# Kernel optimization log

Hardware: AMD Instinct MI355X
Metric: run time of the kernel (lower is better)

## Reference

```python
import jax, jax.numpy as jnp
import numpy as np

# FP4 e2m1 lookup: nibble -> value (bit3 = sign, bits2:0 = e2m1 magnitude)
FP4_LUT = jnp.array([0.0, 0.5, 1.0, 1.5, 2.0, 3.0, 4.0, 6.0,
                     -0.0, -0.5, -1.0, -1.5, -2.0, -3.0, -4.0, -6.0], dtype=jnp.float32)
BLOCK = 16  # elements per micro-scale (one uint8 E8M0 scale per 16 fp4 values)


def _dequant(packed, sf):
    """packed: [R, K//2] int bytes (two fp4 nibbles each, low nibble first).
    sf: [R, K//16] E8M0 exponents (value = 2^(sf-127)). Returns [R, K] f32."""
    R, Kh = packed.shape
    K = Kh * 2
    lo = packed & 0xF
    hi = (packed >> 4) & 0xF
    nib = jnp.stack([lo, hi], axis=-1).reshape(R, K)
    vals = FP4_LUT[nib]  # [R, K]
    block_scale = jnp.exp2((sf - 127).astype(jnp.float32))  # [R, K//16]
    return (vals.reshape(R, K // BLOCK, BLOCK) * block_scale[:, :, None]).reshape(R, K)


def setup_inputs() -> dict:
    key = jax.random.key(0)
    ks = jax.random.split(key, 6)
    M, N, K = 8192, 4096, 4224  # K = in_features(4096) + select_num(128)
    A_packed = jax.random.randint(ks[0], (M, K // 2), 0, 256, dtype=jnp.int32)
    SFA = jax.random.randint(ks[1], (M, K // BLOCK), 118, 134, dtype=jnp.int32)
    B_packed = jax.random.randint(ks[2], (N, K // 2), 0, 256, dtype=jnp.int32)
    SFB = jax.random.randint(ks[3], (N, K // BLOCK), 118, 134, dtype=jnp.int32)
    scale = jax.random.uniform(ks[4], (1,), dtype=jnp.float32, minval=0.5, maxval=1.5)
    bias = jax.random.normal(ks[5], (N,), dtype=jnp.float32)
    return {"A_packed": A_packed, "SFA": SFA, "scale": scale,
            "B_packed": B_packed, "SFB": SFB, "bias": bias}


def reference(A_packed, SFA, scale, B_packed, SFB, bias):
    A = _dequant(A_packed, SFA)        # [M, K]
    B = _dequant(B_packed, SFB)        # [N, K]
    # y = scale * (A @ B^T) + bias   (self.scale == 1.0 folded into scale)
    y = scale[0] * jnp.einsum('mk,nk->mn', A, B) + bias[None, :]
    return y
```

## Files before the change

kernel.cpp:

```cpp
#include <hip/hip_runtime.h>
#include <stdint.h>

#define M_DIM 8192
#define N_DIM 4096
#define K_DIM 4224
#define BK 64

typedef float f32x16 __attribute__((ext_vector_type(16)));
typedef int   i32x8  __attribute__((ext_vector_type(8)));
typedef int   i32x4  __attribute__((ext_vector_type(4)));

#define RAW_BARRIER()  asm volatile("s_barrier" ::: "memory")
#define WAIT_VM4()     asm volatile("s_waitcnt vmcnt(4)" ::: "memory")
#define WAIT_VM0()     asm volatile("s_waitcnt vmcnt(0)" ::: "memory")

__device__ __forceinline__ uint32_t conv4(uint32_t x, uint32_t k1) {
    uint32_t n7   = x & 0x07070707u;
    uint32_t base = __builtin_amdgcn_perm(0x46444240u, 0x3E3C3800u, n7);
    uint32_t nz   = __builtin_amdgcn_perm(0x01010101u, 0x01010100u, n7);
    uint32_t sign = (x & 0x08080808u) << 4;
    return (base + nz * k1 - (nz << 6)) | sign;
}

__global__ __launch_bounds__(256) void dequant_all(
    const int* __restrict__ Ap, const int* __restrict__ SFA, uint8_t* __restrict__ Aout,
    const int* __restrict__ Bp, const int* __restrict__ SFB, uint8_t* __restrict__ Bout)
{
    const int nblkA = M_DIM * K_DIM / 16;
    int i = blockIdx.x * 256 + threadIdx.x;
    const int* p; const int* sf; uint8_t* out; int idx;
    if (i < nblkA) { p = Ap; sf = SFA; out = Aout; idx = i; }
    else           { p = Bp; sf = SFB; out = Bout; idx = i - nblkA; }

    const int4* p4 = (const int4*)p;
    int4 p0 = p4[2 * idx];
    int4 p1 = p4[2 * idx + 1];
    int s4 = (sf[idx] - 127) << 2;
    uint32_t k1 = (uint32_t)(s4 + 64);

    uint32_t o[4];
#pragma unroll
    for (int g = 0; g < 2; ++g) {
        int4 pg = g ? p1 : p0;
        uint32_t w = (uint32_t)(pg.x & 0xFF) | ((uint32_t)(pg.y & 0xFF) << 8) |
                     ((uint32_t)(pg.z & 0xFF) << 16) | ((uint32_t)pg.w << 24);
        uint32_t lr = conv4(w & 0x0F0F0F0Fu, k1);
        uint32_t hr = conv4((w >> 4) & 0x0F0F0F0Fu, k1);
        o[2 * g]     = __builtin_amdgcn_perm(hr, lr, 0x05010400u);
        o[2 * g + 1] = __builtin_amdgcn_perm(hr, lr, 0x07030602u);
    }
    *(uint4*)(out + (size_t)idx * 16) = make_uint4(o[0], o[1], o[2], o[3]);
}

__global__ __launch_bounds__(512, 2) void gemm_mx(
    const uint8_t* __restrict__ A, const uint8_t* __restrict__ B,
    const float* __restrict__ scale, const float* __restrict__ bias,
    float* __restrict__ C)
{
    __shared__ uint8_t smem[98304];

    const int tid  = threadIdx.x;
    const int lane = tid & 63;
    const int w    = tid >> 6;
    const int wm   = w >> 2;
    const int wn   = w & 3;
    const int r31  = lane & 31;
    const int h    = lane >> 5;

    const int lin = blockIdx.y * 16 + blockIdx.x;
    const int o   = (lin & 7) * 64 + (lin >> 3);
    const int bn0 = (o & 15) * 256;
    const int bm0 = (o >> 4) * 256;

    f32x16 acc[4][2];
#pragma unroll
    for (int i = 0; i < 4; ++i)
#pragma unroll
        for (int j = 0; j < 2; ++j)
            acc[i][j] = (f32x16)(0.0f);

    const int srow = lane >> 2;
    const int scol = (((lane & 3) ^ ((lane >> 3) & 3)) << 4);
    const uint8_t* Ag = A + (size_t)(bm0 + w * 32 + srow) * K_DIM + scol;
    const uint8_t* Bg = B + (size_t)(bn0 + w * 32 + srow) * K_DIM + scol;
    uint8_t* Asw = smem + w * 2048;
    uint8_t* Bsw = smem + 16384 + w * 2048;

#define STAGE(koff, boff)                                                        \
    do {                                                                         \
        const uint8_t* ag_ = Ag + (koff);                                        \
        const uint8_t* bg_ = Bg + (koff);                                        \
        __builtin_amdgcn_global_load_lds(                                        \
            (const __attribute__((address_space(1))) void*)(ag_),                \
            (__attribute__((address_space(3))) void*)(Asw + (boff)), 16, 0, 0);  \
        __builtin_amdgcn_global_load_lds(                                        \
            (const __attribute__((address_space(1))) void*)(ag_ + (size_t)16 * K_DIM), \
            (__attribute__((address_space(3))) void*)(Asw + (boff) + 1024), 16, 0, 0); \
        __builtin_amdgcn_global_load_lds(                                        \
            (const __attribute__((address_space(1))) void*)(bg_),                \
            (__attribute__((address_space(3))) void*)(Bsw + (boff)), 16, 0, 0);  \
        __builtin_amdgcn_global_load_lds(                                        \
            (const __attribute__((address_space(1))) void*)(bg_ + (size_t)16 * K_DIM), \
            (__attribute__((address_space(3))) void*)(Bsw + (boff) + 1024), 16, 0, 0); \
    } while (0)

    const int sx = (r31 >> 1) & 3;
    const uint8_t* pa_lo[4]; const uint8_t* pa_hi[4];
    const uint8_t* pb_lo[2]; const uint8_t* pb_hi[2];
#pragma unroll
    for (int mi = 0; mi < 4; ++mi) {
        const uint8_t* base = smem + (wm * 128 + mi * 32 + r31) * 64;
        pa_lo[mi] = base + (((2 * h)     ^ sx) << 4);
        pa_hi[mi] = base + (((2 * h + 1) ^ sx) << 4);
    }
#pragma unroll
    for (int ni = 0; ni < 2; ++ni) {
        const uint8_t* base = smem + 16384 + (wn * 64 + ni * 32 + r31) * 64;
        pb_lo[ni] = base + (((2 * h)     ^ sx) << 4);
        pb_hi[ni] = base + (((2 * h + 1) ^ sx) << 4);
    }

    auto compute = [&](int off) {
        i32x8 af[4], bf[2];
#pragma unroll
        for (int mi = 0; mi < 4; ++mi) {
            i32x4 lo = *(const i32x4*)(pa_lo[mi] + off);
            i32x4 hi = *(const i32x4*)(pa_hi[mi] + off);
            af[mi] = __builtin_shufflevector(lo, hi, 0, 1, 2, 3, 4, 5, 6, 7);
        }
#pragma unroll
        for (int ni = 0; ni < 2; ++ni) {
            i32x4 lo = *(const i32x4*)(pb_lo[ni] + off);
            i32x4 hi = *(const i32x4*)(pb_hi[ni] + off);
            bf[ni] = __builtin_shufflevector(lo, hi, 0, 1, 2, 3, 4, 5, 6, 7);
        }
        __builtin_amdgcn_s_setprio(1);
#pragma unroll
        for (int mi = 0; mi < 4; ++mi)
#pragma unroll
            for (int ni = 0; ni < 2; ++ni)
                acc[mi][ni] = __builtin_amdgcn_mfma_scale_f32_32x32x64_f8f6f4(
                    af[mi], bf[ni], acc[mi][ni],
                    1, 1,
                    0, 0x7F7F7F7F,
                    0, 0x7F7F7F7F);
        __builtin_amdgcn_s_setprio(0);
    };

    STAGE(0 * BK, 0);
    STAGE(1 * BK, 32768);
    WAIT_VM4();
    RAW_BARRIER();

#pragma unroll 1
    for (int g = 0; g < 21; ++g) {
        const int t = 3 * g;
        STAGE((t + 2) * BK, 65536);  compute(0);      WAIT_VM4(); RAW_BARRIER();
        STAGE((t + 3) * BK, 0);      compute(32768);  WAIT_VM4(); RAW_BARRIER();
        STAGE((t + 4) * BK, 32768);  compute(65536);  WAIT_VM4(); RAW_BARRIER();
    }
    STAGE(65 * BK, 65536);  compute(0);      WAIT_VM4(); RAW_BARRIER();
    compute(32768);  WAIT_VM0(); RAW_BARRIER();
    compute(65536);
#undef STAGE

    const float sc = scale[0];
#pragma unroll
    for (int ni = 0; ni < 2; ++ni) {
        const int col = bn0 + wn * 64 + ni * 32 + r31;
        const float bv = bias[col];
#pragma unroll
        for (int mi = 0; mi < 4; ++mi) {
            const int rbase = bm0 + wm * 128 + mi * 32 + 4 * h;
#pragma unroll
            for (int reg = 0; reg < 16; ++reg) {
                const int row = rbase + (reg & 3) + 8 * (reg >> 2);
                C[(size_t)row * N_DIM + col] = sc * acc[mi][ni][reg] + bv;
            }
        }
    }
}

extern "C" void kernel_launch(void* const* d_in, const int* in_sizes, int n_in,
                              void* d_out, int out_size, void* d_ws, size_t ws_size,
                              hipStream_t stream) {
    const int*   A_packed = (const int*)d_in[0];
    const int*   SFA      = (const int*)d_in[1];
    const float* scale    = (const float*)d_in[2];
    const int*   B_packed = (const int*)d_in[3];
    const int*   SFB      = (const int*)d_in[4];
    const float* bias     = (const float*)d_in[5];
    float*       out      = (float*)d_out;

    uint8_t* Abf8 = (uint8_t*)d_ws;
    uint8_t* Bbf8 = Abf8 + (size_t)M_DIM * K_DIM;

    const int nblkA = M_DIM * K_DIM / 16;
    const int nblkB = N_DIM * K_DIM / 16;
    dequant_all<<<(nblkA + nblkB) / 256, 256, 0, stream>>>(
        A_packed, SFA, Abf8, B_packed, SFB, Bbf8);

    dim3 grid(N_DIM / 256, M_DIM / 256);
    gemm_mx<<<grid, 512, 0, stream>>>(Abf8, Bbf8, scale, bias, out);
}
```

Before: 346.8 us.

## Deepen LDS ring to four stages and prefetch MFMA fragments across iterations

The shared-memory ring grows from three to four 32KB stages so global loads run one more K-step ahead. LDS fragment reads for the next K-step are interleaved with the current step's MFMAs using double-buffered register fragments, to hide LDS latency behind matrix work. The cost is 128KB of LDS per block, which may limit the launch bound of two blocks per CU, plus higher register pressure from the extra fragment buffers.

```diff
diff --git a/kernel.cpp b/kernel.cpp
--- a/kernel.cpp
+++ b/kernel.cpp
@@ -57,7 +57,7 @@
     const float* __restrict__ scale, const float* __restrict__ bias,
     float* __restrict__ C)
 {
-    __shared__ uint8_t smem[98304];
+    __shared__ uint8_t smem[131072];
 
     const int tid  = threadIdx.x;
     const int lane = tid & 63;
@@ -120,48 +120,73 @@
         pb_hi[ni] = base + (((2 * h + 1) ^ sx) << 4);
     }
 
-    auto compute = [&](int off) {
-        i32x8 af[4], bf[2];
-#pragma unroll
-        for (int mi = 0; mi < 4; ++mi) {
-            i32x4 lo = *(const i32x4*)(pa_lo[mi] + off);
-            i32x4 hi = *(const i32x4*)(pa_hi[mi] + off);
-            af[mi] = __builtin_shufflevector(lo, hi, 0, 1, 2, 3, 4, 5, 6, 7);
-        }
-#pragma unroll
-        for (int ni = 0; ni < 2; ++ni) {
-            i32x4 lo = *(const i32x4*)(pb_lo[ni] + off);
-            i32x4 hi = *(const i32x4*)(pb_hi[ni] + off);
-            bf[ni] = __builtin_shufflevector(lo, hi, 0, 1, 2, 3, 4, 5, 6, 7);
-        }
-        __builtin_amdgcn_s_setprio(1);
-#pragma unroll
-        for (int mi = 0; mi < 4; ++mi)
-#pragma unroll
-            for (int ni = 0; ni < 2; ++ni)
-                acc[mi][ni] = __builtin_amdgcn_mfma_scale_f32_32x32x64_f8f6f4(
-                    af[mi], bf[ni], acc[mi][ni],
-                    1, 1,
-                    0, 0x7F7F7F7F,
-                    0, 0x7F7F7F7F);
-        __builtin_amdgcn_s_setprio(0);
+    i32x8 afX0[2], afX1[2], bfX0[2], bfX1[2], afY[2];
+
+    auto rd = [&](const uint8_t* plo, const uint8_t* phi, int off, i32x8& dst) {
+        i32x4 lo = *(const i32x4*)(plo + off);
+        i32x4 hi = *(const i32x4*)(phi + off);
+        dst = __builtin_shufflevector(lo, hi, 0, 1, 2, 3, 4, 5, 6, 7);
     };
+    auto mm = [&](const i32x8& a, const i32x8& b, f32x16& c) {
+        c = __builtin_amdgcn_mfma_scale_f32_32x32x64_f8f6f4(
+                a, b, c, 1, 1, 0, 0x7F7F7F7F, 0, 0x7F7F7F7F);
+    };
+
+#define CORE(AC, BC, AN, BN, OB0, OB1)                        \
+    rd(pa_lo[2], pa_hi[2], OB0, afY[0]);                      \
+    rd(pa_lo[3], pa_hi[3], OB0, afY[1]);                      \
+    __builtin_amdgcn_s_setprio(1);                            \
+    mm(AC[0], BC[0], acc[0][0]); mm(AC[0], BC[1], acc[0][1]); \
+    mm(AC[1], BC[0], acc[1][0]); mm(AC[1], BC[1], acc[1][1]); \
+    __builtin_amdgcn_s_setprio(0);                            \
+    rd(pa_lo[0], pa_hi[0], OB1, AN[0]);                       \
+    rd(pa_lo[1], pa_hi[1], OB1, AN[1]);                       \
+    rd(pb_lo[0], pb_hi[0], OB1, BN[0]);                       \
+    rd(pb_lo[1], pb_hi[1], OB1, BN[1]);                       \
+    __builtin_amdgcn_s_setprio(1);                            \
+    mm(afY[0], BC[0], acc[2][0]); mm(afY[0], BC[1], acc[2][1]); \
+    mm(afY[1], BC[0], acc[3][0]); mm(afY[1], BC[1], acc[3][1]); \
+    __builtin_amdgcn_s_setprio(0);
+
+#define BODY(T, AC, BC, AN, BN, OB0, OB1, OB3)                \
+    STAGE(((T) + 3) * BK, OB3);                               \
+    CORE(AC, BC, AN, BN, OB0, OB1)                            \
+    WAIT_VM4(); RAW_BARRIER();
 
     STAGE(0 * BK, 0);
     STAGE(1 * BK, 32768);
+    STAGE(2 * BK, 65536);
     WAIT_VM4();
     RAW_BARRIER();
+    rd(pa_lo[0], pa_hi[0], 0, afX0[0]);
+    rd(pa_lo[1], pa_hi[1], 0, afX0[1]);
+    rd(pb_lo[0], pb_hi[0], 0, bfX0[0]);
+    rd(pb_lo[1], pb_hi[1], 0, bfX0[1]);
 
 #pragma unroll 1
-    for (int g = 0; g < 21; ++g) {
-        const int t = 3 * g;
-        STAGE((t + 2) * BK, 65536);  compute(0);      WAIT_VM4(); RAW_BARRIER();
-        STAGE((t + 3) * BK, 0);      compute(32768);  WAIT_VM4(); RAW_BARRIER();
-        STAGE((t + 4) * BK, 32768);  compute(65536);  WAIT_VM4(); RAW_BARRIER();
-    }
-    STAGE(65 * BK, 65536);  compute(0);      WAIT_VM4(); RAW_BARRIER();
-    compute(32768);  WAIT_VM0(); RAW_BARRIER();
-    compute(65536);
+    for (int g = 0; g < 15; ++g) {
+        const int t = 4 * g;
+        BODY(t,     afX0, bfX0, afX1, bfX1, 0,     32768, 98304)
+        BODY(t + 1, afX1, bfX1, afX0, bfX0, 32768, 65536, 0)
+        BODY(t + 2, afX0, bfX0, afX1, bfX1, 65536, 98304, 32768)
+        BODY(t + 3, afX1, bfX1, afX0, bfX0, 98304, 0,     65536)
+    }
+    BODY(60, afX0, bfX0, afX1, bfX1, 0,     32768, 98304)
+    BODY(61, afX1, bfX1, afX0, bfX0, 32768, 65536, 0)
+    BODY(62, afX0, bfX0, afX1, bfX1, 65536, 98304, 32768)
+    CORE(afX1, bfX1, afX0, bfX0, 98304, 0)
+    WAIT_VM0(); RAW_BARRIER();
+    CORE(afX0, bfX0, afX1, bfX1, 0, 32768)
+    rd(pa_lo[2], pa_hi[2], 32768, afY[0]);
+    rd(pa_lo[3], pa_hi[3], 32768, afY[1]);
+    __builtin_amdgcn_s_setprio(1);
+    mm(afX1[0], bfX1[0], acc[0][0]); mm(afX1[0], bfX1[1], acc[0][1]);
+    mm(afX1[1], bfX1[0], acc[1][0]); mm(afX1[1], bfX1[1], acc[1][1]);
+    mm(afY[0],  bfX1[0], acc[2][0]); mm(afY[0],  bfX1[1], acc[2][1]);
+    mm(afY[1],  bfX1[0], acc[3][0]); mm(afY[1],  bfX1[1], acc[3][1]);
+    __builtin_amdgcn_s_setprio(0);
+#undef BODY
+#undef CORE
 #undef STAGE
 
     const float sc = scale[0];
```

New measurement: 346.2 us. No clear change (-0.2%).
